# Performance work log

Measured on AMD Instinct MI355X. Metric: run time of the kernel, lower is better.

The kernel has to match this reference:

```python
import jax, jax.numpy as jnp
import numpy as np

B, S, D = 1, 4096, 1024
H, G = 16, 4
DK = D // H            # 64, per-head dim
HKV = H // G           # 4 KV heads
DKV = D // G           # 256, KV projection width
SCALE = 1.0 / np.sqrt(np.float32(DK))


def setup_inputs() -> dict:
    key = jax.random.key(0)
    ks = jax.random.split(key, 10)
    std = 0.02
    return {
        "x": jax.random.normal(ks[0], (B, S, D), jnp.float32),
        "mask": jax.random.bernoulli(ks[1], 0.1, (B, 1, S)),  # True = masked out
        "Wq": jax.random.normal(ks[2], (D, D), jnp.float32) * std,
        "bq": jnp.zeros((D,), jnp.float32),
        "Wk": jax.random.normal(ks[3], (D, DKV), jnp.float32) * std,
        "bk": jnp.zeros((DKV,), jnp.float32),
        "Wv": jax.random.normal(ks[4], (D, DKV), jnp.float32) * std,
        "bv": jnp.zeros((DKV,), jnp.float32),
        "Wo": jax.random.normal(ks[5], (D, D), jnp.float32) * std,
        "bo": jnp.zeros((D,), jnp.float32),
    }


def reference(x, mask, Wq, bq, Wk, bk, Wv, bv, Wo, bo):
    b, s, _ = x.shape
    # projections
    q = (x @ Wq + bq).reshape(b, s, H, DK).transpose(0, 2, 1, 3)      # [B,H,S,DK]
    k = (x @ Wk + bk).reshape(b, s, HKV, DK).transpose(0, 2, 1, 3)    # [B,HKV,S,DK]
    v = (x @ Wv + bv).reshape(b, s, HKV, DK).transpose(0, 2, 1, 3)    # [B,HKV,S,DK]
    # expand KV heads: head h = kv_head * G + g (matches torch expand+reshape)
    k = jnp.repeat(k, G, axis=1)                                       # [B,H,S,DK]
    v = jnp.repeat(v, G, axis=1)                                       # [B,H,S,DK]
    scores = jnp.einsum("bhsd,bhtd->bhst", q, k) * SCALE              # [B,H,S,S]
    neg_inf = jnp.finfo(scores.dtype).min
    scores = jnp.where(mask[:, None, :, :], neg_inf, scores)           # mask: [B,1,1,S]
    attn = jax.nn.softmax(scores, axis=-1)
    out = jnp.einsum("bhst,bhtd->bhsd", attn, v)                      # [B,H,S,DK]
    out = out.transpose(0, 2, 1, 3).reshape(b, s, D)
    return out @ Wo + bo
```

## Files before the change

### kernel.cpp

```cpp
#include <hip/hip_runtime.h>
#include <cstdint>
#include <cstddef>

#define S_LEN 4096
#define DMODEL 1024
#define NHEADS 16
#define HDK 64
#define DKV 256
#define NTOT 1536
#define QSCALE 0.18033688011112042f

typedef __bf16 bf16;
typedef __bf16 bf16x8 __attribute__((ext_vector_type(8)));
typedef float f32x4 __attribute__((ext_vector_type(4)));

typedef __attribute__((address_space(3))) void lds_void;
typedef const __attribute__((address_space(1))) void gbl_void;

__device__ __forceinline__ void gload16(const void* g, void* l) {
  __builtin_amdgcn_global_load_lds((gbl_void*)g, (lds_void*)l, 16, 0, 0);
}

__global__ __launch_bounds__(256) void prep(
    const float* __restrict__ x, const int* __restrict__ mask,
    const float* __restrict__ Wq, const float* __restrict__ Wk,
    const float* __restrict__ Wv, const float* __restrict__ Wo,
    bf16* __restrict__ xb, float* __restrict__ mkf, bf16* __restrict__ mkb,
    bf16* __restrict__ Wqt, bf16* __restrict__ Wkt,
    bf16* __restrict__ Wvt, bf16* __restrict__ Wot) {
  const int z = blockIdx.z;
  if (z < 4) {
    const float* src;
    bf16* dst;
    int C;
    switch (z) {
      case 0: src = Wq; dst = Wqt; C = DMODEL; break;
      case 1: src = Wk; dst = Wkt; C = DKV; break;
      case 2: src = Wv; dst = Wvt; C = DKV; break;
      default: src = Wo; dst = Wot; C = DMODEL; break;
    }
    const int c0 = blockIdx.x * 32;
    if (c0 >= C) return;
    __shared__ float tile[32][33];
    const int tx = threadIdx.x & 31;
    const int ty = threadIdx.x >> 5;
    const int r0 = blockIdx.y * 32;
#pragma unroll
    for (int i = 0; i < 4; i++)
      tile[ty + i * 8][tx] = src[(size_t)(r0 + ty + i * 8) * C + c0 + tx];
    __syncthreads();
#pragma unroll
    for (int i = 0; i < 4; i++)
      dst[(size_t)(c0 + ty + i * 8) * DMODEL + r0 + tx] = (bf16)tile[tx][ty + i * 8];
  } else {
    const int b = blockIdx.y * 32 + blockIdx.x;
    const int half = z - 4;
    const int i = ((half * 1024 + b) * 256 + (int)threadIdx.x) * 8;
    float4 a = *(const float4*)(x + i);
    float4 c = *(const float4*)(x + i + 4);
    bf16 o[8] = {(bf16)a.x, (bf16)a.y, (bf16)a.z, (bf16)a.w,
                 (bf16)c.x, (bf16)c.y, (bf16)c.z, (bf16)c.w};
    *(uint4*)(xb + i) = *(uint4*)o;
    if (half == 1 && b < 2) {
      const int mi = (b * 256 + (int)threadIdx.x) * 8;
#pragma unroll
      for (int j = 0; j < 8; j++) {
        float keep = mask[mi + j] ? 0.0f : 1.0f;
        mkf[mi + j] = keep;
        mkb[mi + j] = (bf16)keep;
      }
    }
  }
}

template <int QKV>
__global__ __launch_bounds__(256) void gemm_ld(
    const bf16* __restrict__ A, const bf16* __restrict__ Bt, int M, int N, int K,
    int NT,
    const float* __restrict__ bq, const float* __restrict__ bk,
    const float* __restrict__ bv, const float* __restrict__ mkf,
    bf16* __restrict__ Qb, bf16* __restrict__ Kb, bf16* __restrict__ Vtb,
    const float* __restrict__ bo, float* __restrict__ Co) {
  __shared__ bf16 As[64 * 64];
  __shared__ bf16 Bs[128 * 64];
  const int t = threadIdx.x;
  const int lane = t & 63;
  const int wave = t >> 6;

  const int bid = blockIdx.x;
  const int xcd = bid & 7;
  const int local = bid >> 3;
  const int m_local = local / NT;
  const int ntile = local - m_local * NT;
  const int mchunk = (M >> 6) >> 3;
  const int m0 = (xcd * mchunk + m_local) * 64;
  const int n0 = ntile * 128;

  const int wm = (wave >> 1) * 32;
  const int wn = (wave & 1) * 64;
  const int lr = lane & 15;
  const int quad = lane >> 4;

  const int sr = lane >> 3;
  const int sc = ((lane & 7) ^ (lane >> 3)) * 8;

  f32x4 acc[2][4] = {};

  for (int k0 = 0; k0 < K; k0 += 64) {
    __syncthreads();
#pragma unroll
    for (int j = 0; j < 2; j++) {
      const int rbase = wave * 16 + j * 8;
      gload16(A + (size_t)(m0 + rbase + sr) * K + k0 + sc, &As[rbase * 64]);
    }
#pragma unroll
    for (int j = 0; j < 4; j++) {
      const int rbase = wave * 32 + j * 8;
      gload16(Bt + (size_t)(n0 + rbase + sr) * K + k0 + sc, &Bs[rbase * 64]);
    }
    __syncthreads();
#pragma unroll
    for (int kh2 = 0; kh2 < 2; kh2++) {
      const int fo = ((kh2 * 4 + quad) ^ (lr & 7)) * 8;
      bf16x8 af[2], bfr[4];
#pragma unroll
      for (int mt = 0; mt < 2; mt++)
        af[mt] = *(const bf16x8*)(&As[(wm + mt * 16 + lr) * 64 + fo]);
#pragma unroll
      for (int nt = 0; nt < 4; nt++)
        bfr[nt] = *(const bf16x8*)(&Bs[(wn + nt * 16 + lr) * 64 + fo]);
#pragma unroll
      for (int mt = 0; mt < 2; mt++)
#pragma unroll
        for (int nt = 0; nt < 4; nt++)
          acc[mt][nt] = __builtin_amdgcn_mfma_f32_16x16x32_bf16(af[mt], bfr[nt], acc[mt][nt], 0, 0, 0);
    }
  }

#pragma unroll
  for (int nt = 0; nt < 4; nt++) {
    const int n = n0 + wn + nt * 16 + lr;
    if (QKV) {
      if (n < DMODEL) {
        const float b = bq[n];
#pragma unroll
        for (int mt = 0; mt < 2; mt++)
#pragma unroll
          for (int r = 0; r < 4; r++) {
            const int m = m0 + wm + mt * 16 + quad * 4 + r;
            Qb[(size_t)m * DMODEL + n] = (bf16)((acc[mt][nt][r] + b) * QSCALE);
          }
      } else if (n < DMODEL + DKV) {
        const float b = bk[n - DMODEL];
#pragma unroll
        for (int mt = 0; mt < 2; mt++)
#pragma unroll
          for (int r = 0; r < 4; r++) {
            const int m = m0 + wm + mt * 16 + quad * 4 + r;
            Kb[(size_t)m * DKV + (n - DMODEL)] = (bf16)(acc[mt][nt][r] + b);
          }
      } else {
        const float b = bv[n - DMODEL - DKV];
#pragma unroll
        for (int mt = 0; mt < 2; mt++)
#pragma unroll
          for (int r = 0; r < 4; r++) {
            const int m = m0 + wm + mt * 16 + quad * 4 + r;
            Vtb[(size_t)(n - DMODEL - DKV) * S_LEN + m] = (bf16)((acc[mt][nt][r] + b) * mkf[m]);
          }
      }
    } else {
      const float b = bo[n];
#pragma unroll
      for (int mt = 0; mt < 2; mt++)
#pragma unroll
        for (int r = 0; r < 4; r++) {
          const int m = m0 + wm + mt * 16 + quad * 4 + r;
          Co[(size_t)m * N + n] = acc[mt][nt][r] + b;
        }
    }
  }
}

__global__ __launch_bounds__(256) void flash_attn(
    const bf16* __restrict__ Q, const bf16* __restrict__ K,
    const bf16* __restrict__ Vt, const bf16* __restrict__ mkb,
    bf16* __restrict__ O) {
  const int h = blockIdx.y;
  const int kvh = h >> 2;
  const int q0 = blockIdx.x * 128;
  const int t = threadIdx.x;
  const int lane = t & 63;
  const int wave = t >> 6;
  const int lr = lane & 15;
  const int quad = lane >> 4;

  __shared__ bf16 Ks[2][128 * 64];
  __shared__ bf16 Vs[2][64 * 128];
  __shared__ bf16 Ps[4][32][36];

  bf16x8 aq[2][2];
#pragma unroll
  for (int qt = 0; qt < 2; qt++) {
    const int qrow = q0 + wave * 32 + qt * 16 + lr;
    aq[qt][0] = *(const bf16x8*)(Q + (size_t)qrow * DMODEL + h * HDK + quad * 8);
    aq[qt][1] = *(const bf16x8*)(Q + (size_t)qrow * DMODEL + h * HDK + 32 + quad * 8);
  }

  const bf16* Kg = K + kvh * HDK;
  const bf16* Vg = Vt + (size_t)kvh * HDK * S_LEN;
  const int krl = lane >> 3;
  const int kgc = ((lane & 7) ^ (lane >> 3)) * 8;
  const int vrl = lane >> 4;

#pragma unroll
  for (int j = 0; j < 4; j++) {
    const int rb = wave * 32 + j * 8;
    gload16(Kg + (size_t)(rb + krl) * DKV + kgc, &Ks[0][rb * 64]);
  }
#pragma unroll
  for (int j = 0; j < 4; j++) {
    const int rb = wave * 16 + j * 4;
    const int g = ((lane & 15) ^ (j * 4 + vrl)) * 8;
    gload16(Vg + (size_t)(rb + vrl) * S_LEN + g, &Vs[0][rb * 128]);
  }

  f32x4 o_acc[2][4] = {};
  f32x4 l_acc[2] = {};
  int buf = 0;

  for (int kv0 = 0; kv0 < S_LEN; kv0 += 128) {
    __syncthreads();
    const int kvn = kv0 + 128;
    if (kvn < S_LEN) {
      const int nb = buf ^ 1;
#pragma unroll
      for (int j = 0; j < 4; j++) {
        const int rb = wave * 32 + j * 8;
        gload16(Kg + (size_t)(kvn + rb + krl) * DKV + kgc, &Ks[nb][rb * 64]);
      }
#pragma unroll
      for (int j = 0; j < 4; j++) {
        const int rb = wave * 16 + j * 4;
        const int g = ((lane & 15) ^ (j * 4 + vrl)) * 8;
        gload16(Vg + (size_t)(rb + vrl) * S_LEN + kvn + g, &Vs[nb][rb * 128]);
      }
    }
    const bf16* Ksb = Ks[buf];
    const bf16* Vsb = Vs[buf];

#pragma unroll
    for (int kc = 0; kc < 4; kc++) {
      bf16x8 ak[2][2];
#pragma unroll
      for (int ntl = 0; ntl < 2; ntl++) {
        const int krow = kc * 32 + ntl * 16 + lr;
        ak[ntl][0] = *(const bf16x8*)(&Ksb[krow * 64 + ((quad) ^ (lr & 7)) * 8]);
        ak[ntl][1] = *(const bf16x8*)(&Ksb[krow * 64 + ((4 + quad) ^ (lr & 7)) * 8]);
      }
#pragma unroll
      for (int qt = 0; qt < 2; qt++) {
#pragma unroll
        for (int ntl = 0; ntl < 2; ntl++) {
          f32x4 s = {};
          s = __builtin_amdgcn_mfma_f32_16x16x32_bf16(ak[ntl][0], aq[qt][0], s, 0, 0, 0);
          s = __builtin_amdgcn_mfma_f32_16x16x32_bf16(ak[ntl][1], aq[qt][1], s, 0, 0, 0);
          bf16 p4[4];
#pragma unroll
          for (int r = 0; r < 4; r++) p4[r] = (bf16)__builtin_amdgcn_exp2f(s[r]);
          *(uint2*)(&Ps[wave][qt * 16 + lr][ntl * 16 + quad * 4]) = *(uint2*)p4;
        }
      }
      bf16x8 bvf[4];
#pragma unroll
      for (int ntv = 0; ntv < 4; ntv++) {
        const int vrow = ntv * 16 + lr;
        bvf[ntv] = *(const bf16x8*)(&Vsb[vrow * 128 + ((kc * 4 + quad) ^ lr) * 8]);
      }
      const bf16x8 mkfv = *(const bf16x8*)(mkb + kv0 + kc * 32 + quad * 8);
#pragma unroll
      for (int qt = 0; qt < 2; qt++) {
        bf16x8 ap = *(const bf16x8*)(&Ps[wave][qt * 16 + lr][quad * 8]);
#pragma unroll
        for (int ntv = 0; ntv < 4; ntv++)
          o_acc[qt][ntv] = __builtin_amdgcn_mfma_f32_16x16x32_bf16(ap, bvf[ntv], o_acc[qt][ntv], 0, 0, 0);
        l_acc[qt] = __builtin_amdgcn_mfma_f32_16x16x32_bf16(ap, mkfv, l_acc[qt], 0, 0, 0);
      }
    }
    buf ^= 1;
  }

#pragma unroll
  for (int qt = 0; qt < 2; qt++) {
#pragma unroll
    for (int ntv = 0; ntv < 4; ntv++) {
#pragma unroll
      for (int r = 0; r < 4; r++) {
        const int row = q0 + wave * 32 + qt * 16 + quad * 4 + r;
        O[(size_t)row * DMODEL + h * HDK + ntv * 16 + lr] =
            (bf16)(o_acc[qt][ntv][r] / l_acc[qt][r]);
      }
    }
  }
}

extern "C" void kernel_launch(void* const* d_in, const int* in_sizes, int n_in,
                              void* d_out, int out_size, void* d_ws, size_t ws_size,
                              hipStream_t stream) {
  const float* x = (const float*)d_in[0];
  const int* mask = (const int*)d_in[1];
  const float* Wq = (const float*)d_in[2];
  const float* bq = (const float*)d_in[3];
  const float* Wk = (const float*)d_in[4];
  const float* bk = (const float*)d_in[5];
  const float* Wv = (const float*)d_in[6];
  const float* bv = (const float*)d_in[7];
  const float* Wo = (const float*)d_in[8];
  const float* bo = (const float*)d_in[9];
  float* out = (float*)d_out;

  char* w = (char*)d_ws;
  bf16* xb  = (bf16*)w; w += (size_t)S_LEN * DMODEL * 2;
  bf16* Wqt = (bf16*)w; w += (size_t)DMODEL * DMODEL * 2;
  bf16* Wkt = (bf16*)w; w += (size_t)DKV * DMODEL * 2;
  bf16* Wvt = (bf16*)w; w += (size_t)DKV * DMODEL * 2;
  bf16* Wot = (bf16*)w; w += (size_t)DMODEL * DMODEL * 2;
  bf16* Qb  = (bf16*)w; w += (size_t)S_LEN * DMODEL * 2;
  bf16* Kb  = (bf16*)w; w += (size_t)S_LEN * DKV * 2;
  bf16* Vtb = (bf16*)w; w += (size_t)DKV * S_LEN * 2;
  bf16* Ob  = (bf16*)w; w += (size_t)S_LEN * DMODEL * 2;
  float* mkf = (float*)w; w += (size_t)S_LEN * 4;
  bf16* mkb = (bf16*)w; w += (size_t)S_LEN * 2;

  prep<<<dim3(32, 32, 6), 256, 0, stream>>>(
      x, mask, Wq, Wk, Wv, Wo, xb, mkf, mkb, Wqt, Wkt, Wvt, Wot);

  gemm_ld<1><<<dim3((S_LEN / 64) * (NTOT / 128)), 256, 0, stream>>>(
      xb, Wqt, S_LEN, NTOT, DMODEL, NTOT / 128, bq, bk, bv, mkf, Qb, Kb, Vtb,
      nullptr, nullptr);

  flash_attn<<<dim3(S_LEN / 128, NHEADS), 256, 0, stream>>>(Qb, Kb, Vtb, mkb, Ob);

  gemm_ld<0><<<dim3((S_LEN / 64) * (DMODEL / 128)), 256, 0, stream>>>(
      Ob, Wot, S_LEN, DMODEL, DMODEL, DMODEL / 128, nullptr, nullptr, nullptr,
      nullptr, nullptr, nullptr, nullptr, bo, out);
}
```

Before: 214.7 us.

## Split attention KV range across two blocks and stage V transpose through LDS

```diff
diff --git a/kernel.cpp b/kernel.cpp
--- a/kernel.cpp
+++ b/kernel.cpp
@@ -137,6 +137,31 @@
     }
   }
 
+  if (QKV && n0 >= DMODEL + DKV) {
+    __syncthreads();
+#pragma unroll
+    for (int nt = 0; nt < 4; nt++) {
+      const int nrel = wn + nt * 16 + lr;
+      const float b = bv[n0 - DMODEL - DKV + nrel];
+#pragma unroll
+      for (int mt = 0; mt < 2; mt++)
+#pragma unroll
+        for (int r = 0; r < 4; r++) {
+          const int mrel = wm + mt * 16 + quad * 4 + r;
+          Bs[nrel * 64 + mrel] = (bf16)((acc[mt][nt][r] + b) * mkf[m0 + mrel]);
+        }
+    }
+    __syncthreads();
+    const int row = t >> 1;
+    const int hh = (t & 1) * 32;
+#pragma unroll
+    for (int j = 0; j < 4; j++) {
+      *(uint4*)(Vtb + (size_t)(n0 - DMODEL - DKV + row) * S_LEN + m0 + hh + j * 8) =
+          *(const uint4*)(&Bs[row * 64 + hh + j * 8]);
+    }
+    return;
+  }
+
 #pragma unroll
   for (int nt = 0; nt < 4; nt++) {
     const int n = n0 + wn + nt * 16 + lr;
@@ -150,7 +175,7 @@
             const int m = m0 + wm + mt * 16 + quad * 4 + r;
             Qb[(size_t)m * DMODEL + n] = (bf16)((acc[mt][nt][r] + b) * QSCALE);
           }
-      } else if (n < DMODEL + DKV) {
+      } else {
         const float b = bk[n - DMODEL];
 #pragma unroll
         for (int mt = 0; mt < 2; mt++)
@@ -159,15 +184,6 @@
             const int m = m0 + wm + mt * 16 + quad * 4 + r;
             Kb[(size_t)m * DKV + (n - DMODEL)] = (bf16)(acc[mt][nt][r] + b);
           }
-      } else {
-        const float b = bv[n - DMODEL - DKV];
-#pragma unroll
-        for (int mt = 0; mt < 2; mt++)
-#pragma unroll
-          for (int r = 0; r < 4; r++) {
-            const int m = m0 + wm + mt * 16 + quad * 4 + r;
-            Vtb[(size_t)(n - DMODEL - DKV) * S_LEN + m] = (bf16)((acc[mt][nt][r] + b) * mkf[m]);
-          }
       }
     } else {
       const float b = bo[n];
@@ -185,18 +201,20 @@
 __global__ __launch_bounds__(256) void flash_attn(
     const bf16* __restrict__ Q, const bf16* __restrict__ K,
     const bf16* __restrict__ Vt, const bf16* __restrict__ mkb,
-    bf16* __restrict__ O) {
+    float* __restrict__ op, float* __restrict__ lp) {
   const int h = blockIdx.y;
   const int kvh = h >> 2;
-  const int q0 = blockIdx.x * 128;
+  const int q0 = (blockIdx.x >> 1) * 128;
+  const int half = blockIdx.x & 1;
+  const int kvbase = half * (S_LEN / 2);
   const int t = threadIdx.x;
   const int lane = t & 63;
   const int wave = t >> 6;
   const int lr = lane & 15;
   const int quad = lane >> 4;
 
-  __shared__ bf16 Ks[2][128 * 64];
-  __shared__ bf16 Vs[2][64 * 128];
+  __shared__ bf16 Ks[128 * 64];
+  __shared__ bf16 Vs[64 * 128];
   __shared__ bf16 Ps[4][32][36];
 
   bf16x8 aq[2][2];
@@ -213,41 +231,23 @@
   const int kgc = ((lane & 7) ^ (lane >> 3)) * 8;
   const int vrl = lane >> 4;
 
-#pragma unroll
-  for (int j = 0; j < 4; j++) {
-    const int rb = wave * 32 + j * 8;
-    gload16(Kg + (size_t)(rb + krl) * DKV + kgc, &Ks[0][rb * 64]);
-  }
-#pragma unroll
-  for (int j = 0; j < 4; j++) {
-    const int rb = wave * 16 + j * 4;
-    const int g = ((lane & 15) ^ (j * 4 + vrl)) * 8;
-    gload16(Vg + (size_t)(rb + vrl) * S_LEN + g, &Vs[0][rb * 128]);
-  }
-
   f32x4 o_acc[2][4] = {};
   f32x4 l_acc[2] = {};
-  int buf = 0;
-
-  for (int kv0 = 0; kv0 < S_LEN; kv0 += 128) {
-    __syncthreads();
-    const int kvn = kv0 + 128;
-    if (kvn < S_LEN) {
-      const int nb = buf ^ 1;
-#pragma unroll
-      for (int j = 0; j < 4; j++) {
-        const int rb = wave * 32 + j * 8;
-        gload16(Kg + (size_t)(kvn + rb + krl) * DKV + kgc, &Ks[nb][rb * 64]);
-      }
-#pragma unroll
-      for (int j = 0; j < 4; j++) {
-        const int rb = wave * 16 + j * 4;
-        const int g = ((lane & 15) ^ (j * 4 + vrl)) * 8;
-        gload16(Vg + (size_t)(rb + vrl) * S_LEN + kvn + g, &Vs[nb][rb * 128]);
-      }
-    }
-    const bf16* Ksb = Ks[buf];
-    const bf16* Vsb = Vs[buf];
+
+  for (int kv0 = kvbase; kv0 < kvbase + S_LEN / 2; kv0 += 128) {
+    __syncthreads();
+#pragma unroll
+    for (int j = 0; j < 4; j++) {
+      const int rb = wave * 32 + j * 8;
+      gload16(Kg + (size_t)(kv0 + rb + krl) * DKV + kgc, &Ks[rb * 64]);
+    }
+#pragma unroll
+    for (int j = 0; j < 4; j++) {
+      const int rb = wave * 16 + j * 4;
+      const int g = ((lane & 15) ^ (j * 4 + vrl)) * 8;
+      gload16(Vg + (size_t)(rb + vrl) * S_LEN + kv0 + g, &Vs[rb * 128]);
+    }
+    __syncthreads();
 
 #pragma unroll
     for (int kc = 0; kc < 4; kc++) {
@@ -255,8 +255,8 @@
 #pragma unroll
       for (int ntl = 0; ntl < 2; ntl++) {
         const int krow = kc * 32 + ntl * 16 + lr;
-        ak[ntl][0] = *(const bf16x8*)(&Ksb[krow * 64 + ((quad) ^ (lr & 7)) * 8]);
-        ak[ntl][1] = *(const bf16x8*)(&Ksb[krow * 64 + ((4 + quad) ^ (lr & 7)) * 8]);
+        ak[ntl][0] = *(const bf16x8*)(&Ks[krow * 64 + ((quad) ^ (lr & 7)) * 8]);
+        ak[ntl][1] = *(const bf16x8*)(&Ks[krow * 64 + ((4 + quad) ^ (lr & 7)) * 8]);
       }
 #pragma unroll
       for (int qt = 0; qt < 2; qt++) {
@@ -275,7 +275,7 @@
 #pragma unroll
       for (int ntv = 0; ntv < 4; ntv++) {
         const int vrow = ntv * 16 + lr;
-        bvf[ntv] = *(const bf16x8*)(&Vsb[vrow * 128 + ((kc * 4 + quad) ^ lr) * 8]);
+        bvf[ntv] = *(const bf16x8*)(&Vs[vrow * 128 + ((kc * 4 + quad) ^ lr) * 8]);
       }
       const bf16x8 mkfv = *(const bf16x8*)(mkb + kv0 + kc * 32 + quad * 8);
 #pragma unroll
@@ -287,21 +287,42 @@
         l_acc[qt] = __builtin_amdgcn_mfma_f32_16x16x32_bf16(ap, mkfv, l_acc[qt], 0, 0, 0);
       }
     }
-    buf ^= 1;
-  }
-
+  }
+
+  float* opb = op + (size_t)half * S_LEN * DMODEL;
 #pragma unroll
   for (int qt = 0; qt < 2; qt++) {
 #pragma unroll
-    for (int ntv = 0; ntv < 4; ntv++) {
-#pragma unroll
-      for (int r = 0; r < 4; r++) {
-        const int row = q0 + wave * 32 + qt * 16 + quad * 4 + r;
-        O[(size_t)row * DMODEL + h * HDK + ntv * 16 + lr] =
-            (bf16)(o_acc[qt][ntv][r] / l_acc[qt][r]);
-      }
-    }
-  }
+    for (int r = 0; r < 4; r++) {
+      const int row = q0 + wave * 32 + qt * 16 + quad * 4 + r;
+#pragma unroll
+      for (int ntv = 0; ntv < 4; ntv++)
+        opb[(size_t)row * DMODEL + h * HDK + ntv * 16 + lr] = o_acc[qt][ntv][r];
+      if (lr == 0) lp[((size_t)half * S_LEN + row) * NHEADS + h] = l_acc[qt][r];
+    }
+  }
+}
+
+__global__ __launch_bounds__(256) void combine(
+    const float* __restrict__ op, const float* __restrict__ lp,
+    bf16* __restrict__ Ob) {
+  const int i = (blockIdx.x * 256 + (int)threadIdx.x) * 8;
+  const int row = i >> 10;
+  const int h = (i & 1023) >> 6;
+  const float l = lp[(size_t)row * NHEADS + h] +
+                  lp[((size_t)S_LEN + row) * NHEADS + h];
+  const float inv = 1.0f / l;
+  const float* p0 = op + i;
+  const float* p1 = op + (size_t)S_LEN * DMODEL + i;
+  float4 a0 = *(const float4*)(p0);
+  float4 a1 = *(const float4*)(p0 + 4);
+  float4 b0 = *(const float4*)(p1);
+  float4 b1 = *(const float4*)(p1 + 4);
+  bf16 o[8] = {(bf16)((a0.x + b0.x) * inv), (bf16)((a0.y + b0.y) * inv),
+               (bf16)((a0.z + b0.z) * inv), (bf16)((a0.w + b0.w) * inv),
+               (bf16)((a1.x + b1.x) * inv), (bf16)((a1.y + b1.y) * inv),
+               (bf16)((a1.z + b1.z) * inv), (bf16)((a1.w + b1.w) * inv)};
+  *(uint4*)(Ob + i) = *(uint4*)o;
 }
 
 extern "C" void kernel_launch(void* const* d_in, const int* in_sizes, int n_in,
@@ -331,6 +352,9 @@
   bf16* Ob  = (bf16*)w; w += (size_t)S_LEN * DMODEL * 2;
   float* mkf = (float*)w; w += (size_t)S_LEN * 4;
   bf16* mkb = (bf16*)w; w += (size_t)S_LEN * 2;
+  w = (char*)(((uintptr_t)w + 255) & ~(uintptr_t)255);
+  float* op = (float*)w; w += (size_t)2 * S_LEN * DMODEL * 4;
+  float* lp = (float*)w; w += (size_t)2 * S_LEN * NHEADS * 4;
 
   prep<<<dim3(32, 32, 6), 256, 0, stream>>>(
       x, mask, Wq, Wk, Wv, Wo, xb, mkf, mkb, Wqt, Wkt, Wvt, Wot);
@@ -339,7 +363,9 @@
       xb, Wqt, S_LEN, NTOT, DMODEL, NTOT / 128, bq, bk, bv, mkf, Qb, Kb, Vtb,
       nullptr, nullptr);
 
-  flash_attn<<<dim3(S_LEN / 128, NHEADS), 256, 0, stream>>>(Qb, Kb, Vtb, mkb, Ob);
+  flash_attn<<<dim3((S_LEN / 128) * 2, NHEADS), 256, 0, stream>>>(
+      Qb, Kb, Vtb, mkb, op, lp);
+  combine<<<dim3(S_LEN * DMODEL / (256 * 8)), 256, 0, stream>>>(op, lp, Ob);
 
   gemm_ld<0><<<dim3((S_LEN / 64) * (DMODEL / 128)), 256, 0, stream>>>(
       Ob, Wot, S_LEN, DMODEL, DMODEL, DMODEL / 128, nullptr, nullptr, nullptr,
```

New measurement: 227.3 us. 1.06x slower.
